# Kernel optimization log

Measured on AMD Instinct MI355X. Metric: run time of the kernel, lower is better.

## Reference

```python
import jax, jax.numpy as jnp
import numpy as np

NEG_INF = -9e15
ALPHA = 0.2  # attention leaky_relu slope


def _gat_layer(h, adj_mask, W, a1, a2):
    # h: [N, Fin], W: [Fin, D], a1/a2: [D]
    Wh = h @ W                                   # [N, D]
    f1 = Wh @ a1                                 # [N]
    f2 = Wh @ a2                                 # [N]
    e = jax.nn.leaky_relu(f1[:, None] + f2[None, :], ALPHA)  # [N, N]
    scores = jnp.where(adj_mask, e, NEG_INF)
    att = jax.nn.softmax(scores, axis=-1)        # row-normalized over neighbors
    return att @ Wh                              # [N, D]


def setup_inputs() -> dict:
    key = jax.random.key(0)
    ks = jax.random.split(key, 12)
    N, Fin, H, D, C = 4096, 512, 8, 64, 64
    s = 0.1
    x = jax.random.normal(ks[0], (N, Fin), jnp.float32)
    adj = jax.random.randint(ks[1], (N, N), 0, 2, jnp.int32)
    W = jax.random.normal(ks[2], (H, Fin, D), jnp.float32) * s
    a1 = jax.random.normal(ks[3], (H, D), jnp.float32) * s
    a2 = jax.random.normal(ks[4], (H, D), jnp.float32) * s
    Wo = jax.random.normal(ks[5], (H * D, C), jnp.float32) * s
    ao1 = jax.random.normal(ks[6], (C,), jnp.float32) * s
    ao2 = jax.random.normal(ks[7], (C,), jnp.float32) * s
    W1 = jax.random.normal(ks[8], (512, N), jnp.float32) * 0.01  # nn.Linear(N, 512)
    b1 = jnp.zeros((512,), jnp.float32)
    W2 = jax.random.normal(ks[9], (256, 512), jnp.float32) * 0.04  # nn.Linear(512, 256)
    b2 = jnp.zeros((256,), jnp.float32)
    return {"x": x, "adj": adj, "W": W, "a1": a1, "a2": a2,
            "Wo": Wo, "ao1": ao1, "ao2": ao2,
            "W1": W1, "b1": b1, "W2": W2, "b2": b2}


def reference(x, adj, W, a1, a2, Wo, ao1, ao2, W1, b1, W2, b2):
    mask = adj > 0                                    # [N, N]
    # multi-head dense attention, concat=True -> ELU per head
    heads = jax.vmap(lambda Wk, a1k, a2k: _gat_layer(x, mask, Wk, a1k, a2k))(W, a1, a2)  # [H, N, D]
    h = jax.nn.elu(heads).transpose(1, 0, 2).reshape(x.shape[0], -1)  # [N, H*D]
    # output attention layer, concat=False (no inner ELU), then outer ELU
    out = jax.nn.elu(_gat_layer(h, mask, Wo, ao1, ao2))  # [N, C]
    out = jax.nn.log_softmax(out, axis=0)                # over nodes (dim=0)
    # MLP head on transposed features: [C, N] -> [C, 512] -> [C, 256]
    y = jax.nn.leaky_relu(out.T @ W1.T + b1, 0.1)
    y = y @ W2.T + b2
    return y
```

## Files before the change

### kernel.cpp

```cpp
#include <hip/hip_runtime.h>
#include <hip/hip_bf16.h>
#include <math.h>


#define N_NODES 4096
#define FIN 512
#define NHEAD 8
#define DHEAD 64
#define NCLS 64
#define NW 64

typedef unsigned short u16;
typedef unsigned long long u64;
typedef __attribute__((ext_vector_type(8))) short bf16x8;
typedef __attribute__((ext_vector_type(4))) float f32x4;

__device__ __forceinline__ float lrelu02(float x) { return x > 0.f ? x : 0.2f * x; }
__device__ __forceinline__ u16 bf16u(float x) {
    __hip_bfloat16 h = __float2bfloat16(x);
    return __builtin_bit_cast(unsigned short, h);
}
__device__ __forceinline__ f32x4 mfma16(bf16x8 a, bf16x8 b, f32x4 c) {
    return __builtin_amdgcn_mfma_f32_16x16x32_bf16(a, b, c, 0, 0, 0);
}
__device__ __forceinline__ unsigned fkey(float f) {
    unsigned u = __builtin_bit_cast(unsigned, f);
    return (u & 0x80000000u) ? ~u : (u | 0x80000000u);
}
__device__ __forceinline__ float funkey(unsigned k) {
    unsigned u = (k & 0x80000000u) ? (k ^ 0x80000000u) : ~k;
    return __builtin_bit_cast(float, u);
}

__global__ void pack_mask(const int* __restrict__ adj, u64* __restrict__ mb,
                          unsigned* __restrict__ gmk) {
    if (blockIdx.x == 0 && threadIdx.x < 16) gmk[threadIdx.x] = 0u;
    int nwaves = (gridDim.x * blockDim.x) >> 6;
    int wid = (blockIdx.x * blockDim.x + threadIdx.x) >> 6;
    int lane = threadIdx.x & 63;
    for (int w = wid; w < N_NODES * NW; w += nwaves) {
        int i = w >> 6, wc = w & 63;
        int j = (wc << 6) | lane;
        u64 m = __ballot(adj[(size_t)i * N_NODES + j] > 0);
        if (lane == 0) mb[w] = m;
    }
}

__global__ void cvt4(const float* __restrict__ s, u16* __restrict__ d, int n4) {
    int i = blockIdx.x * blockDim.x + threadIdx.x;
    if (i < n4) {
        float4 v = ((const float4*)s)[i];
        ushort4 o = {bf16u(v.x), bf16u(v.y), bf16u(v.z), bf16u(v.w)};
        ((ushort4*)d)[i] = o;
    }
}

__global__ __launch_bounds__(256) void to_bf16_T(
    const float* __restrict__ src, int ldsrc, size_t cstep,
    u16* __restrict__ dst, size_t dstep, int ldd) {
    __shared__ alignas(16) u16 T[64][72];
    const int j0 = blockIdx.x * 64;
    const size_t c0 = (size_t)blockIdx.y * cstep;
    u16* d = dst + (size_t)blockIdx.y * dstep;
    const int t = threadIdx.x;
    const int row = t & 63, g = t >> 6;
    #pragma unroll
    for (int k = 0; k < 16; k += 4) {
        float4 v = *(const float4*)(src + (size_t)(j0 + row) * ldsrc + c0 + g * 16 + k);
        T[g * 16 + k + 0][row] = bf16u(v.x);
        T[g * 16 + k + 1][row] = bf16u(v.y);
        T[g * 16 + k + 2][row] = bf16u(v.z);
        T[g * 16 + k + 3][row] = bf16u(v.w);
    }
    __syncthreads();
    const int dd = t >> 2, jc = (t & 3) * 16;
    *(uint4*)(d + (size_t)dd * ldd + j0 + jc) = *(const uint4*)&T[dd][jc];
    *(uint4*)(d + (size_t)dd * ldd + j0 + jc + 8) = *(const uint4*)&T[dd][jc + 8];
}

__global__ __launch_bounds__(256) void gemm_fused(
    const u16* __restrict__ A, int lda, const u16* __restrict__ Bt, int ldb,
    const float* __restrict__ a1a, const float* __restrict__ a2a,
    u16* __restrict__ WhBT, float* __restrict__ f1o, float* __restrict__ f2o,
    unsigned* __restrict__ gmk, int K) {
    __shared__ alignas(16) u16 T[64][72];
    const int t = threadIdx.x, lane = t & 63, wv = t >> 6;
    const int c16 = lane & 15, kg = lane >> 4;
    const int h = blockIdx.x;
    const int bm = blockIdx.y * 64;
    const u16* Ap = A + (size_t)(bm + wv * 16 + c16) * lda + kg * 8;
    const u16* Bp = Bt + (size_t)(h * 64 + c16) * ldb + kg * 8;
    f32x4 acc[4] = {};
    #pragma unroll 4
    for (int k0 = 0; k0 < K; k0 += 32) {
        bf16x8 a = *(const bf16x8*)(Ap + k0);
        #pragma unroll
        for (int ct = 0; ct < 4; ++ct) {
            bf16x8 b = *(const bf16x8*)(Bp + (size_t)ct * 16 * ldb + k0);
            acc[ct] = mfma16(a, b, acc[ct]);
        }
    }
    float a1v[4], a2v[4];
    #pragma unroll
    for (int ct = 0; ct < 4; ++ct) {
        a1v[ct] = a1a[h * 64 + ct * 16 + c16];
        a2v[ct] = a2a[h * 64 + ct * 16 + c16];
    }
    float mx = -1e30f;
    #pragma unroll
    for (int r = 0; r < 4; ++r) {
        float s1 = 0.f, s2 = 0.f;
        int rl = wv * 16 + kg * 4 + r;
        #pragma unroll
        for (int ct = 0; ct < 4; ++ct) {
            float v = acc[ct][r];
            s1 = fmaf(v, a1v[ct], s1);
            s2 = fmaf(v, a2v[ct], s2);
            T[ct * 16 + c16][rl] = bf16u(v);
        }
        #pragma unroll
        for (int off = 1; off < 16; off <<= 1) {
            s1 += __shfl_xor(s1, off, 64);
            s2 += __shfl_xor(s2, off, 64);
        }
        if (c16 == 0) {
            f1o[(size_t)h * N_NODES + bm + rl] = s1;
            f2o[(size_t)h * N_NODES + bm + rl] = s2;
        }
        mx = fmaxf(mx, s2);
    }
    mx = fmaxf(mx, __shfl_xor(mx, 16, 64));
    mx = fmaxf(mx, __shfl_xor(mx, 32, 64));
    if (lane == 0) atomicMax(&gmk[h], fkey(mx));
    __syncthreads();
    const int dd = t >> 2, jc = (t & 3) * 16;
    u16* dst = WhBT + (size_t)(h * 64 + dd) * N_NODES + bm;
    *(uint4*)(dst + jc) = *(const uint4*)&T[dd][jc];
    *(uint4*)(dst + jc + 8) = *(const uint4*)&T[dd][jc + 8];
}

__global__ void coefk(const float* __restrict__ f1, const float* __restrict__ f2,
                      const unsigned* __restrict__ gmk, float4* __restrict__ rowc,
                      float2* __restrict__ uv) {
    int h = blockIdx.y;
    int i = blockIdx.x * 256 + threadIdx.x;
    float g = funkey(gmk[h]);
    float a = f1[(size_t)h * N_NODES + i];
    float s = a + g;
    float M = lrelu02(s);
    rowc[(size_t)h * N_NODES + i] = make_float4(__expf(s - M), __expf(0.2f * s - M), 0.f, 0.f);
    float b = f2[(size_t)h * N_NODES + i] - g;
    uv[(size_t)h * N_NODES + i] = make_float2(__expf(b), __expf(0.2f * b));
}

template <int NH, int ROWS, int JSPLIT, int OUTF>
__global__ __launch_bounds__(256) void attn_v3(
    const u16* __restrict__ WhB, const float2* __restrict__ uv,
    const float4* __restrict__ rowc, const u64* __restrict__ mb,
    float* __restrict__ outp, float* __restrict__ denP) {
    constexpr int NQ = ROWS / 4;
    constexpr int NMT = ROWS / 16;
    constexpr int NJT = (N_NODES / 64) / JSPLIT;
    __shared__ alignas(16) u16 pS[2][ROWS][64];
    __shared__ float Tof[(OUTF == 3) ? 64 * 33 : 1];
    const int b = blockIdx.x;
    int h, ib, js;
    if (NH == 8) { h = b & 7; int r = b >> 3; js = r % JSPLIT; ib = r / JSPLIT; }
    else { h = 0; js = b % JSPLIT; ib = b / JSPLIT; }
    const int i0 = ib * ROWS;
    const int jt0 = js * NJT;
    const int t = threadIdx.x, lane = t & 63, wv = t >> 6;
    const int wv_u = __builtin_amdgcn_readfirstlane(wv);

    const float2* __restrict__ uvp = uv + (size_t)h * N_NODES;
    const float4* __restrict__ rcp = rowc + (size_t)h * N_NODES;
    const u64* __restrict__ mbp = mb + (size_t)(i0 + wv_u) * NW + jt0;

    float Aq[NQ], Bq[NQ], den[NQ];
    #pragma unroll
    for (int q = 0; q < NQ; ++q) {
        float4 rc = rcp[i0 + q * 4 + wv];
        Aq[q] = rc.x; Bq[q] = rc.y; den[q] = 0.f;
    }
    const int wcE = lane ^ (wv << 3);
    const int wcO = lane ^ ((wv + 4) << 3);
    const int kg = lane >> 4, c16 = lane & 15;
    const int ocol = wv * 16 + c16;
    const u16* bptr = WhB + ((size_t)h * 64 + ocol) * N_NODES + jt0 * 64 + kg * 8;
    const int sw8 = (c16 & 7) << 3;
    f32x4 acc[NMT] = {};

    bf16x8 b0 = *(const bf16x8*)(bptr);
    bf16x8 b1 = *(const bf16x8*)(bptr + 32);
    float2 uvv = uvp[jt0 * 64 + lane];
    u64 m[NQ];
    #pragma unroll
    for (int q = 0; q < NQ; ++q) m[q] = mbp[q * 4 * NW];

    for (int it = 0; it < NJT; ++it) {
        const int buf = it & 1;
        const int nit = (it + 1 < NJT) ? it + 1 : it;
        bf16x8 nb0 = *(const bf16x8*)(bptr + (size_t)nit * 64);
        bf16x8 nb1 = *(const bf16x8*)(bptr + (size_t)nit * 64 + 32);
        float2 nuv = uvp[(jt0 + nit) * 64 + lane];
        u64 nm[NQ];
        #pragma unroll
        for (int q = 0; q < NQ; ++q) nm[q] = mbp[q * 4 * NW + nit];
        #pragma unroll
        for (int q = 0; q < NQ; ++q) {
            unsigned wlo = __builtin_amdgcn_readfirstlane((unsigned)m[q]);
            unsigned whi = __builtin_amdgcn_readfirstlane((unsigned)(m[q] >> 32));
            u64 ws = ((u64)whi << 32) | wlo;
            float tv = fmaxf(Aq[q] * uvv.x, Bq[q] * uvv.y);
            float p;
            asm("v_cndmask_b32 %0, 0, %1, %2" : "=v"(p) : "v"(tv), "s"(ws));
            den[q] += p;
            pS[buf][q * 4 + wv][(q & 1) ? wcO : wcE] = bf16u(p);
        }
        __syncthreads();
        __builtin_amdgcn_s_setprio(1);
        #pragma unroll
        for (int mt = 0; mt < NMT; ++mt) {
            const u16* ap = &pS[buf][mt * 16 + c16][0];
            bf16x8 a0 = *(const bf16x8*)&ap[(kg * 8) ^ sw8];
            bf16x8 a1 = *(const bf16x8*)&ap[(32 + kg * 8) ^ sw8];
            acc[mt] = mfma16(a0, b0, acc[mt]);
            acc[mt] = mfma16(a1, b1, acc[mt]);
        }
        __builtin_amdgcn_s_setprio(0);
        b0 = nb0; b1 = nb1; uvv = nuv;
        #pragma unroll
        for (int q = 0; q < NQ; ++q) m[q] = nm[q];
    }

    #pragma unroll
    for (int q = 0; q < NQ; ++q) {
        float s = den[q];
        #pragma unroll
        for (int off = 32; off; off >>= 1) s += __shfl_xor(s, off, 64);
        den[q] = s;
    }

    if constexpr (OUTF == 1) {
        if (lane == 0) {
            #pragma unroll
            for (int q = 0; q < NQ; ++q)
                denP[(size_t)js * (8 * N_NODES) + (size_t)h * N_NODES + i0 + q * 4 + wv] = den[q];
        }
        float* dst = outp + (size_t)js * N_NODES * 512;
        #pragma unroll
        for (int mt = 0; mt < NMT; ++mt)
            #pragma unroll
            for (int r = 0; r < 4; ++r)
                dst[(size_t)(i0 + mt * 16 + kg * 4 + r) * 512 + h * 64 + ocol] = acc[mt][r];
    } else {
        if (lane == 0) {
            #pragma unroll
            for (int q = 0; q < NQ; ++q)
                denP[(size_t)js * N_NODES + i0 + q * 4 + wv] = den[q];
        }
        #pragma unroll
        for (int mt = 0; mt < NMT; ++mt)
            #pragma unroll
            for (int r = 0; r < 4; ++r)
                Tof[ocol * 33 + mt * 16 + kg * 4 + r] = acc[mt][r];
        __syncthreads();
        const int c = t >> 2, r0 = (t & 3) * 8;
        float* dst = outp + (size_t)js * 64 * N_NODES + (size_t)c * N_NODES + i0 + r0;
        float4 v0 = {Tof[c * 33 + r0 + 0], Tof[c * 33 + r0 + 1],
                     Tof[c * 33 + r0 + 2], Tof[c * 33 + r0 + 3]};
        float4 v1 = {Tof[c * 33 + r0 + 4], Tof[c * 33 + r0 + 5],
                     Tof[c * 33 + r0 + 6], Tof[c * 33 + r0 + 7]};
        *(float4*)(dst) = v0;
        *(float4*)(dst + 4) = v1;
    }
}

__global__ __launch_bounds__(256) void combine8(
    const float* __restrict__ part, const float* __restrict__ denp,
    u16* __restrict__ hB) {
    const int t4 = (blockIdx.x * 256 + threadIdx.x) * 4;
    const int i = t4 >> 9, c = t4 & 511, h = c >> 6;
    float4 p0 = *(const float4*)(part + t4);
    float4 p1 = *(const float4*)(part + (size_t)N_NODES * 512 + t4);
    float d = denp[h * N_NODES + i] + denp[8 * N_NODES + h * N_NODES + i];
    float inv = d > 0.f ? 1.f / d : 0.f;
    float v[4] = {(p0.x + p1.x) * inv, (p0.y + p1.y) * inv,
                  (p0.z + p1.z) * inv, (p0.w + p1.w) * inv};
    ushort4 o;
    #pragma unroll
    for (int k = 0; k < 4; ++k) {
        float e = v[k] > 0.f ? v[k] : expm1f(v[k]);
        ((u16*)&o)[k] = bf16u(e);
    }
    *(ushort4*)(hB + t4) = o;
}

__global__ __launch_bounds__(256) void combine1_lsm(
    const float* __restrict__ partT, const float* __restrict__ denp,
    u16* __restrict__ lsT) {
    __shared__ float vb[N_NODES];
    __shared__ float r[256];
    const int c = blockIdx.x, t = threadIdx.x;
    float m = -1e30f;
    for (int i = t * 4; i < N_NODES; i += 1024) {
        float4 s = {0.f, 0.f, 0.f, 0.f}, d = {0.f, 0.f, 0.f, 0.f};
        #pragma unroll
        for (int js = 0; js < 4; ++js) {
            float4 pv = *(const float4*)(partT + (size_t)js * 64 * N_NODES +
                                         (size_t)c * N_NODES + i);
            float4 dv = *(const float4*)(denp + (size_t)js * N_NODES + i);
            s.x += pv.x; s.y += pv.y; s.z += pv.z; s.w += pv.w;
            d.x += dv.x; d.y += dv.y; d.z += dv.z; d.w += dv.w;
        }
        float vv[4] = {d.x > 0.f ? s.x / d.x : 0.f, d.y > 0.f ? s.y / d.y : 0.f,
                       d.z > 0.f ? s.z / d.z : 0.f, d.w > 0.f ? s.w / d.w : 0.f};
        #pragma unroll
        for (int k = 0; k < 4; ++k) {
            float e = vv[k] > 0.f ? vv[k] : expm1f(vv[k]);
            vb[i + k] = e;
            m = fmaxf(m, e);
        }
    }
    r[t] = m;
    __syncthreads();
    for (int s = 128; s; s >>= 1) {
        if (t < s) r[t] = fmaxf(r[t], r[t + s]);
        __syncthreads();
    }
    m = r[0];
    __syncthreads();
    float sum = 0.f;
    for (int i = t; i < N_NODES; i += 256) sum += __expf(vb[i] - m);
    r[t] = sum;
    __syncthreads();
    for (int s = 128; s; s >>= 1) {
        if (t < s) r[t] += r[t + s];
        __syncthreads();
    }
    float lse = m + __logf(r[0]);
    for (int i = t * 4; i < N_NODES; i += 1024) {
        ushort4 o = {bf16u(vb[i] - lse), bf16u(vb[i + 1] - lse),
                     bf16u(vb[i + 2] - lse), bf16u(vb[i + 3] - lse)};
        *(ushort4*)(lsT + (size_t)c * N_NODES + i) = o;
    }
}

__global__ __launch_bounds__(256) void mlp1_mfma(
    const u16* __restrict__ lsT, const u16* __restrict__ W1B,
    float* __restrict__ part) {
    const int t = threadIdx.x, lane = t & 63, wv = t >> 6;
    const int c16 = lane & 15, kg = lane >> 4;
    const int ks = blockIdx.x & 15;
    const int bn = (blockIdx.x >> 4) * 64;
    const int kb = ks * 256;
    const u16* Ap = lsT + (size_t)(wv * 16 + c16) * N_NODES + kb + kg * 8;
    const u16* Bp = W1B + (size_t)(bn + c16) * N_NODES + kb + kg * 8;
    f32x4 acc[4] = {};
    #pragma unroll
    for (int k0 = 0; k0 < 256; k0 += 32) {
        bf16x8 a = *(const bf16x8*)(Ap + k0);
        #pragma unroll
        for (int ct = 0; ct < 4; ++ct) {
            bf16x8 b = *(const bf16x8*)(Bp + (size_t)ct * 16 * N_NODES + k0);
            acc[ct] = mfma16(a, b, acc[ct]);
        }
    }
    float* dst = part + (size_t)ks * 64 * 512;
    #pragma unroll
    for (int ct = 0; ct < 4; ++ct)
        #pragma unroll
        for (int r = 0; r < 4; ++r)
            dst[(size_t)(wv * 16 + kg * 4 + r) * 512 + bn + ct * 16 + c16] = acc[ct][r];
}

__global__ void mlp1_fin(const float* __restrict__ part, const float* __restrict__ b1,
                         float* __restrict__ y1) {
    int idx = blockIdx.x * 256 + threadIdx.x;
    int o = idx & 511;
    float s = 0.f;
    #pragma unroll
    for (int ks = 0; ks < 16; ++ks) s += part[(size_t)ks * 32768 + idx];
    s += b1[o];
    y1[idx] = s > 0.f ? s : 0.1f * s;
}

__global__ __launch_bounds__(256) void mlp2(
    const float* __restrict__ y1, const float* __restrict__ W2,
    const float* __restrict__ b2, float* __restrict__ out) {
    __shared__ alignas(16) float row[512];
    int c = blockIdx.x, t = threadIdx.x;
    row[t] = y1[(size_t)c * 512 + t];
    row[t + 256] = y1[(size_t)c * 512 + t + 256];
    __syncthreads();
    float acc = 0.f;
    #pragma unroll 4
    for (int o = 0; o < 512; o += 4) {
        float4 w4 = *(const float4*)(W2 + (size_t)t * 512 + o);
        float4 r4 = *(const float4*)(&row[o]);
        acc += w4.x * r4.x + w4.y * r4.y + w4.z * r4.z + w4.w * r4.w;
    }
    out[(size_t)c * 256 + t] = acc + b2[t];
}

extern "C" void kernel_launch(void* const* d_in, const int* in_sizes, int n_in,
                              void* d_out, int out_size, void* d_ws, size_t ws_size,
                              hipStream_t stream) {
    const float* x   = (const float*)d_in[0];
    const int*   adj = (const int*)d_in[1];
    const float* W   = (const float*)d_in[2];
    const float* a1  = (const float*)d_in[3];
    const float* a2  = (const float*)d_in[4];
    const float* Wo  = (const float*)d_in[5];
    const float* ao1 = (const float*)d_in[6];
    const float* ao2 = (const float*)d_in[7];
    const float* W1  = (const float*)d_in[8];
    const float* b1  = (const float*)d_in[9];
    const float* W2  = (const float*)d_in[10];
    const float* b2  = (const float*)d_in[11];
    float* out = (float*)d_out;

    char* ws = (char*)d_ws;
    size_t off = 0;
    auto alloc = [&](size_t bytes) {
        void* p = ws + off;
        off += (bytes + 255) & ~(size_t)255;
        return p;
    };
    u64*     mb     = (u64*)alloc((size_t)N_NODES * NW * 8);
    u16*     xB     = (u16*)alloc((size_t)N_NODES * FIN * 2);
    u16*     WBt    = (u16*)alloc((size_t)NHEAD * DHEAD * FIN * 2);
    u16*     WoBt   = (u16*)alloc((size_t)DHEAD * FIN * 2);
    u16*     W1B    = (u16*)alloc((size_t)512 * N_NODES * 2);
    u16*     WhB    = (u16*)alloc((size_t)NHEAD * DHEAD * N_NODES * 2);
    u16*     WhoB   = (u16*)alloc((size_t)DHEAD * N_NODES * 2);
    u16*     hB     = (u16*)alloc((size_t)N_NODES * 512 * 2);
    float*   part8  = (float*)alloc((size_t)2 * N_NODES * 512 * 4);
    float*   den8   = (float*)alloc((size_t)2 * 8 * N_NODES * 4);
    float*   partT1 = (float*)alloc((size_t)4 * 64 * N_NODES * 4);
    float*   den1   = (float*)alloc((size_t)4 * N_NODES * 4);
    u16*     lsT    = (u16*)alloc((size_t)64 * N_NODES * 2);
    float*   part   = (float*)alloc((size_t)16 * 64 * 512 * 4);
    float*   f1b    = (float*)alloc((size_t)9 * N_NODES * 4);
    float*   f2b    = (float*)alloc((size_t)9 * N_NODES * 4);
    unsigned* gmk   = (unsigned*)alloc(16 * 4);
    float4*  rowc   = (float4*)alloc((size_t)9 * N_NODES * 16);
    float2*  uvb    = (float2*)alloc((size_t)9 * N_NODES * 8);
    float*   y1     = (float*)alloc((size_t)64 * 512 * 4);
    (void)ws_size; (void)in_sizes; (void)n_in; (void)out_size;

    pack_mask<<<1024, 256, 0, stream>>>(adj, mb, gmk);
    cvt4<<<(N_NODES * FIN / 4 + 255) / 256, 256, 0, stream>>>(x, xB, N_NODES * FIN / 4);
    cvt4<<<(512 * N_NODES / 4 + 255) / 256, 256, 0, stream>>>(W1, W1B, 512 * N_NODES / 4);
    to_bf16_T<<<dim3(8, 8), 256, 0, stream>>>(W, 64, (size_t)FIN * DHEAD, WBt,
                                              (size_t)DHEAD * FIN, FIN);
    to_bf16_T<<<dim3(8, 1), 256, 0, stream>>>(Wo, 64, 0, WoBt, 0, FIN);
    gemm_fused<<<dim3(8, 64), 256, 0, stream>>>(xB, FIN, WBt, FIN, a1, a2,
                                                WhB, f1b, f2b, gmk, FIN);
    coefk<<<dim3(16, 8), 256, 0, stream>>>(f1b, f2b, gmk, rowc, uvb);
    attn_v3<8, 64, 2, 1><<<(N_NODES / 64) * 2 * 8, 256, 0, stream>>>(
        WhB, uvb, rowc, mb, part8, den8);
    combine8<<<N_NODES * 512 / 4 / 256, 256, 0, stream>>>(part8, den8, hB);
    gemm_fused<<<dim3(1, 64), 256, 0, stream>>>(hB, 512, WoBt, FIN, ao1, ao2,
                                                WhoB, f1b + (size_t)8 * N_NODES,
                                                f2b + (size_t)8 * N_NODES, gmk + 8, FIN);
    coefk<<<dim3(16, 1), 256, 0, stream>>>(f1b + (size_t)8 * N_NODES,
                                           f2b + (size_t)8 * N_NODES, gmk + 8,
                                           rowc + (size_t)8 * N_NODES,
                                           uvb + (size_t)8 * N_NODES);
    attn_v3<1, 32, 4, 3><<<(N_NODES / 32) * 4, 256, 0, stream>>>(
        WhoB, uvb + (size_t)8 * N_NODES, rowc + (size_t)8 * N_NODES, mb, partT1, den1);
    combine1_lsm<<<64, 256, 0, stream>>>(partT1, den1, lsT);
    mlp1_mfma<<<128, 256, 0, stream>>>(lsT, W1B, part);
    mlp1_fin<<<128, 256, 0, stream>>>(part, b1, y1);
    mlp2<<<64, 256, 0, stream>>>(y1, W2, b2, out);
}
```

Before: 209.2 us.

## Widen attention j-tile to 128 with even/odd interleaved mask packing

The adjacency bitmask is repacked into even/odd-column ballots per 128-column tile, so each lane computes two probabilities and writes them to LDS as one packed bf16 pair. The attention kernel processes 128 columns per iteration with four MFMAs per row tile, halving loop and barrier count. Row blocks shrink to 32 for the multi-head pass, and the output layer uses an 8-way j-split with enlarged partial buffers. This trades more blocks and more partial-sum traffic for fewer syncs and wider vector loads.

```diff
diff --git a/kernel.cpp b/kernel.cpp
--- a/kernel.cpp
+++ b/kernel.cpp
@@ -8,7 +8,6 @@
 #define NHEAD 8
 #define DHEAD 64
 #define NCLS 64
-#define NW 64
 
 typedef unsigned short u16;
 typedef unsigned long long u64;
@@ -32,17 +31,27 @@
     return __builtin_bit_cast(float, u);
 }
 
-__global__ void pack_mask(const int* __restrict__ adj, u64* __restrict__ mb,
+__global__ void pack_mask(const int* __restrict__ adj, u64* __restrict__ mb2,
                           unsigned* __restrict__ gmk) {
     if (blockIdx.x == 0 && threadIdx.x < 16) gmk[threadIdx.x] = 0u;
     int nwaves = (gridDim.x * blockDim.x) >> 6;
     int wid = (blockIdx.x * blockDim.x + threadIdx.x) >> 6;
     int lane = threadIdx.x & 63;
-    for (int w = wid; w < N_NODES * NW; w += nwaves) {
-        int i = w >> 6, wc = w & 63;
-        int j = (wc << 6) | lane;
-        u64 m = __ballot(adj[(size_t)i * N_NODES + j] > 0);
-        if (lane == 0) mb[w] = m;
+    const int sl = (2 * lane) & 63;
+    const int slo = (2 * lane + 1) & 63;
+    for (int w = wid; w < N_NODES * 32; w += nwaves) {
+        int i = w >> 5, t128 = w & 31;
+        const int* base = adj + (size_t)i * N_NODES + t128 * 128;
+        int v0 = base[lane];
+        int v1 = base[64 + lane];
+        int e0 = __shfl(v0, sl), e1 = __shfl(v1, sl);
+        int o0 = __shfl(v0, slo), o1 = __shfl(v1, slo);
+        u64 be = __ballot((lane < 32 ? e0 : e1) > 0);
+        u64 bo = __ballot((lane < 32 ? o0 : o1) > 0);
+        if (lane == 0) {
+            mb2[(size_t)w * 2] = be;
+            mb2[(size_t)w * 2 + 1] = bo;
+        }
     }
 }
 
@@ -154,27 +163,27 @@
 }
 
 template <int NH, int ROWS, int JSPLIT, int OUTF>
-__global__ __launch_bounds__(256) void attn_v3(
+__global__ __launch_bounds__(256) void attn_v4(
     const u16* __restrict__ WhB, const float2* __restrict__ uv,
-    const float4* __restrict__ rowc, const u64* __restrict__ mb,
+    const float4* __restrict__ rowc, const u64* __restrict__ mb2,
     float* __restrict__ outp, float* __restrict__ denP) {
     constexpr int NQ = ROWS / 4;
     constexpr int NMT = ROWS / 16;
-    constexpr int NJT = (N_NODES / 64) / JSPLIT;
-    __shared__ alignas(16) u16 pS[2][ROWS][64];
-    __shared__ float Tof[(OUTF == 3) ? 64 * 33 : 1];
+    constexpr int NT = 32 / JSPLIT;
+    __shared__ alignas(16) u16 pS[2][ROWS][128];
+    __shared__ float Tof[(OUTF == 3) ? 64 * (ROWS + 1) : 1];
     const int b = blockIdx.x;
     int h, ib, js;
     if (NH == 8) { h = b & 7; int r = b >> 3; js = r % JSPLIT; ib = r / JSPLIT; }
     else { h = 0; js = b % JSPLIT; ib = b / JSPLIT; }
     const int i0 = ib * ROWS;
-    const int jt0 = js * NJT;
+    const int t0 = js * NT;
     const int t = threadIdx.x, lane = t & 63, wv = t >> 6;
     const int wv_u = __builtin_amdgcn_readfirstlane(wv);
 
     const float2* __restrict__ uvp = uv + (size_t)h * N_NODES;
     const float4* __restrict__ rcp = rowc + (size_t)h * N_NODES;
-    const u64* __restrict__ mbp = mb + (size_t)(i0 + wv_u) * NW + jt0;
+    const u64* __restrict__ mbp = mb2 + (size_t)(i0 + wv_u) * 64 + t0 * 2;
 
     float Aq[NQ], Bq[NQ], den[NQ];
     #pragma unroll
@@ -182,55 +191,68 @@
         float4 rc = rcp[i0 + q * 4 + wv];
         Aq[q] = rc.x; Bq[q] = rc.y; den[q] = 0.f;
     }
-    const int wcE = lane ^ (wv << 3);
-    const int wcO = lane ^ ((wv + 4) << 3);
+    const int wcE = (2 * lane) ^ (wv << 3);
+    const int wcO = (2 * lane) ^ ((wv + 4) << 3);
     const int kg = lane >> 4, c16 = lane & 15;
     const int ocol = wv * 16 + c16;
-    const u16* bptr = WhB + ((size_t)h * 64 + ocol) * N_NODES + jt0 * 64 + kg * 8;
+    const u16* bbase = WhB + ((size_t)h * 64 + ocol) * N_NODES + t0 * 128 + kg * 8;
     const int sw8 = (c16 & 7) << 3;
     f32x4 acc[NMT] = {};
 
-    bf16x8 b0 = *(const bf16x8*)(bptr);
-    bf16x8 b1 = *(const bf16x8*)(bptr + 32);
-    float2 uvv = uvp[jt0 * 64 + lane];
-    u64 m[NQ];
-    #pragma unroll
-    for (int q = 0; q < NQ; ++q) m[q] = mbp[q * 4 * NW];
-
-    for (int it = 0; it < NJT; ++it) {
+    bf16x8 bfr[4];
+    #pragma unroll
+    for (int kc = 0; kc < 4; ++kc) bfr[kc] = *(const bf16x8*)(bbase + kc * 32);
+    float4 uvv = *(const float4*)&uvp[(size_t)t0 * 128 + 2 * lane];
+    u64 me[NQ], mo[NQ];
+    #pragma unroll
+    for (int q = 0; q < NQ; ++q) { me[q] = mbp[q * 256]; mo[q] = mbp[q * 256 + 1]; }
+
+    for (int it = 0; it < NT; ++it) {
         const int buf = it & 1;
-        const int nit = (it + 1 < NJT) ? it + 1 : it;
-        bf16x8 nb0 = *(const bf16x8*)(bptr + (size_t)nit * 64);
-        bf16x8 nb1 = *(const bf16x8*)(bptr + (size_t)nit * 64 + 32);
-        float2 nuv = uvp[(jt0 + nit) * 64 + lane];
-        u64 nm[NQ];
-        #pragma unroll
-        for (int q = 0; q < NQ; ++q) nm[q] = mbp[q * 4 * NW + nit];
+        const int nit = (it + 1 < NT) ? it + 1 : it;
+        bf16x8 nb[4];
+        #pragma unroll
+        for (int kc = 0; kc < 4; ++kc)
+            nb[kc] = *(const bf16x8*)(bbase + (size_t)nit * 128 + kc * 32);
+        float4 nuv = *(const float4*)&uvp[((size_t)t0 + nit) * 128 + 2 * lane];
         #pragma unroll
         for (int q = 0; q < NQ; ++q) {
-            unsigned wlo = __builtin_amdgcn_readfirstlane((unsigned)m[q]);
-            unsigned whi = __builtin_amdgcn_readfirstlane((unsigned)(m[q] >> 32));
-            u64 ws = ((u64)whi << 32) | wlo;
-            float tv = fmaxf(Aq[q] * uvv.x, Bq[q] * uvv.y);
-            float p;
-            asm("v_cndmask_b32 %0, 0, %1, %2" : "=v"(p) : "v"(tv), "s"(ws));
-            den[q] += p;
-            pS[buf][q * 4 + wv][(q & 1) ? wcO : wcE] = bf16u(p);
+            unsigned le = __builtin_amdgcn_readfirstlane((unsigned)me[q]);
+            unsigned he = __builtin_amdgcn_readfirstlane((unsigned)(me[q] >> 32));
+            unsigned lo2 = __builtin_amdgcn_readfirstlane((unsigned)mo[q]);
+            unsigned ho2 = __builtin_amdgcn_readfirstlane((unsigned)(mo[q] >> 32));
+            u64 wse = ((u64)he << 32) | le;
+            u64 wso = ((u64)ho2 << 32) | lo2;
+            float te = fmaxf(Aq[q] * uvv.x, Bq[q] * uvv.y);
+            float to = fmaxf(Aq[q] * uvv.z, Bq[q] * uvv.w);
+            float pe, po;
+            asm("v_cndmask_b32 %0, 0, %1, %2" : "=v"(pe) : "v"(te), "s"(wse));
+            asm("v_cndmask_b32 %0, 0, %1, %2" : "=v"(po) : "v"(to), "s"(wso));
+            den[q] += pe + po;
+            unsigned pk;
+            asm("v_cvt_pk_bf16_f32 %0, %1, %2" : "=v"(pk) : "v"(pe), "v"(po));
+            *(unsigned*)&pS[buf][q * 4 + wv][(q & 1) ? wcO : wcE] = pk;
+        }
+        #pragma unroll
+        for (int q = 0; q < NQ; ++q) {
+            me[q] = mbp[q * 256 + nit * 2];
+            mo[q] = mbp[q * 256 + nit * 2 + 1];
         }
         __syncthreads();
         __builtin_amdgcn_s_setprio(1);
         #pragma unroll
         for (int mt = 0; mt < NMT; ++mt) {
             const u16* ap = &pS[buf][mt * 16 + c16][0];
-            bf16x8 a0 = *(const bf16x8*)&ap[(kg * 8) ^ sw8];
-            bf16x8 a1 = *(const bf16x8*)&ap[(32 + kg * 8) ^ sw8];
-            acc[mt] = mfma16(a0, b0, acc[mt]);
-            acc[mt] = mfma16(a1, b1, acc[mt]);
+            #pragma unroll
+            for (int kc = 0; kc < 4; ++kc) {
+                bf16x8 a = *(const bf16x8*)&ap[(kc * 32 + kg * 8) ^ sw8];
+                acc[mt] = mfma16(a, bfr[kc], acc[mt]);
+            }
         }
         __builtin_amdgcn_s_setprio(0);
-        b0 = nb0; b1 = nb1; uvv = nuv;
-        #pragma unroll
-        for (int q = 0; q < NQ; ++q) m[q] = nm[q];
+        #pragma unroll
+        for (int kc = 0; kc < 4; ++kc) bfr[kc] = nb[kc];
+        uvv = nuv;
     }
 
     #pragma unroll
@@ -263,14 +285,14 @@
         for (int mt = 0; mt < NMT; ++mt)
             #pragma unroll
             for (int r = 0; r < 4; ++r)
-                Tof[ocol * 33 + mt * 16 + kg * 4 + r] = acc[mt][r];
+                Tof[ocol * (ROWS + 1) + mt * 16 + kg * 4 + r] = acc[mt][r];
         __syncthreads();
         const int c = t >> 2, r0 = (t & 3) * 8;
         float* dst = outp + (size_t)js * 64 * N_NODES + (size_t)c * N_NODES + i0 + r0;
-        float4 v0 = {Tof[c * 33 + r0 + 0], Tof[c * 33 + r0 + 1],
-                     Tof[c * 33 + r0 + 2], Tof[c * 33 + r0 + 3]};
-        float4 v1 = {Tof[c * 33 + r0 + 4], Tof[c * 33 + r0 + 5],
-                     Tof[c * 33 + r0 + 6], Tof[c * 33 + r0 + 7]};
+        float4 v0 = {Tof[c * (ROWS + 1) + r0 + 0], Tof[c * (ROWS + 1) + r0 + 1],
+                     Tof[c * (ROWS + 1) + r0 + 2], Tof[c * (ROWS + 1) + r0 + 3]};
+        float4 v1 = {Tof[c * (ROWS + 1) + r0 + 4], Tof[c * (ROWS + 1) + r0 + 5],
+                     Tof[c * (ROWS + 1) + r0 + 6], Tof[c * (ROWS + 1) + r0 + 7]};
         *(float4*)(dst) = v0;
         *(float4*)(dst + 4) = v1;
     }
@@ -306,7 +328,7 @@
     for (int i = t * 4; i < N_NODES; i += 1024) {
         float4 s = {0.f, 0.f, 0.f, 0.f}, d = {0.f, 0.f, 0.f, 0.f};
         #pragma unroll
-        for (int js = 0; js < 4; ++js) {
+        for (int js = 0; js < 8; ++js) {
             float4 pv = *(const float4*)(partT + (size_t)js * 64 * N_NODES +
                                          (size_t)c * N_NODES + i);
             float4 dv = *(const float4*)(denp + (size_t)js * N_NODES + i);
@@ -427,7 +449,7 @@
         off += (bytes + 255) & ~(size_t)255;
         return p;
     };
-    u64*     mb     = (u64*)alloc((size_t)N_NODES * NW * 8);
+    u64*     mb2    = (u64*)alloc((size_t)N_NODES * 64 * 8);
     u16*     xB     = (u16*)alloc((size_t)N_NODES * FIN * 2);
     u16*     WBt    = (u16*)alloc((size_t)NHEAD * DHEAD * FIN * 2);
     u16*     WoBt   = (u16*)alloc((size_t)DHEAD * FIN * 2);
@@ -437,8 +459,8 @@
     u16*     hB     = (u16*)alloc((size_t)N_NODES * 512 * 2);
     float*   part8  = (float*)alloc((size_t)2 * N_NODES * 512 * 4);
     float*   den8   = (float*)alloc((size_t)2 * 8 * N_NODES * 4);
-    float*   partT1 = (float*)alloc((size_t)4 * 64 * N_NODES * 4);
-    float*   den1   = (float*)alloc((size_t)4 * N_NODES * 4);
+    float*   partT1 = (float*)alloc((size_t)8 * 64 * N_NODES * 4);
+    float*   den1   = (float*)alloc((size_t)8 * N_NODES * 4);
     u16*     lsT    = (u16*)alloc((size_t)64 * N_NODES * 2);
     float*   part   = (float*)alloc((size_t)16 * 64 * 512 * 4);
     float*   f1b    = (float*)alloc((size_t)9 * N_NODES * 4);
@@ -449,7 +471,7 @@
     float*   y1     = (float*)alloc((size_t)64 * 512 * 4);
     (void)ws_size; (void)in_sizes; (void)n_in; (void)out_size;
 
-    pack_mask<<<1024, 256, 0, stream>>>(adj, mb, gmk);
+    pack_mask<<<1024, 256, 0, stream>>>(adj, mb2, gmk);
     cvt4<<<(N_NODES * FIN / 4 + 255) / 256, 256, 0, stream>>>(x, xB, N_NODES * FIN / 4);
     cvt4<<<(512 * N_NODES / 4 + 255) / 256, 256, 0, stream>>>(W1, W1B, 512 * N_NODES / 4);
     to_bf16_T<<<dim3(8, 8), 256, 0, stream>>>(W, 64, (size_t)FIN * DHEAD, WBt,
@@ -458,8 +480,8 @@
     gemm_fused<<<dim3(8, 64), 256, 0, stream>>>(xB, FIN, WBt, FIN, a1, a2,
                                                 WhB, f1b, f2b, gmk, FIN);
     coefk<<<dim3(16, 8), 256, 0, stream>>>(f1b, f2b, gmk, rowc, uvb);
-    attn_v3<8, 64, 2, 1><<<(N_NODES / 64) * 2 * 8, 256, 0, stream>>>(
-        WhB, uvb, rowc, mb, part8, den8);
+    attn_v4<8, 32, 2, 1><<<(N_NODES / 32) * 2 * 8, 256, 0, stream>>>(
+        WhB, uvb, rowc, mb2, part8, den8);
     combine8<<<N_NODES * 512 / 4 / 256, 256, 0, stream>>>(part8, den8, hB);
     gemm_fused<<<dim3(1, 64), 256, 0, stream>>>(hB, 512, WoBt, FIN, ao1, ao2,
                                                 WhoB, f1b + (size_t)8 * N_NODES,
@@ -468,8 +490,8 @@
                                            f2b + (size_t)8 * N_NODES, gmk + 8,
                                            rowc + (size_t)8 * N_NODES,
                                            uvb + (size_t)8 * N_NODES);
-    attn_v3<1, 32, 4, 3><<<(N_NODES / 32) * 4, 256, 0, stream>>>(
-        WhoB, uvb + (size_t)8 * N_NODES, rowc + (size_t)8 * N_NODES, mb, partT1, den1);
+    attn_v4<1, 32, 8, 3><<<(N_NODES / 32) * 8, 256, 0, stream>>>(
+        WhoB, uvb + (size_t)8 * N_NODES, rowc + (size_t)8 * N_NODES, mb2, partT1, den1);
     combine1_lsm<<<64, 256, 0, stream>>>(partT1, den1, lsT);
     mlp1_mfma<<<128, 256, 0, stream>>>(lsT, W1B, part);
     mlp1_fin<<<128, 256, 0, stream>>>(part, b1, y1);
```

Measured after the change: 223.1 us. +6.6%, slower.
